# Kernel tuning notes

Hardware: AMD Instinct MI355X
Metric: run time of the kernel (lower is better)

Reference implementation:

```python
import jax, jax.numpy as jnp
import numpy as np

N = 100000      # nodes
E = 1600000     # edges
C = 128         # in_channels == hidden_dim
FP = 512        # fingerprint_dim
L = 3           # num_layers
G = 1024        # number of graphs
W_SCALE = 5.0


def setup_inputs() -> dict:
    key = jax.random.key(0)
    ks = jax.random.split(key, 6)
    x = jax.random.normal(ks[0], (N, C), dtype=jnp.float32)
    Ws = jax.random.normal(ks[1], (L, C, C), dtype=jnp.float32) * W_SCALE
    bs = jnp.zeros((L, C), dtype=jnp.float32)
    Wn = jax.random.normal(ks[2], (L, C, C), dtype=jnp.float32) * W_SCALE
    bn = jnp.zeros((L, C), dtype=jnp.float32)
    Wfp = jax.random.normal(ks[3], (L, FP, C), dtype=jnp.float32) * W_SCALE
    edge_index = jax.random.randint(ks[4], (2, E), 0, N, dtype=jnp.int64)
    batch = jnp.sort(jax.random.randint(ks[5], (N,), 0, G, dtype=jnp.int64))
    return {"x": x, "Ws": Ws, "bs": bs, "Wn": Wn, "bn": bn, "Wfp": Wfp,
            "edge_index": edge_index, "batch": batch}


def reference(x, Ws, bs, Wn, bn, Wfp, edge_index, batch):
    row, col = edge_index[0], edge_index[1]
    fingerprint = jnp.zeros((G, FP), dtype=x.dtype)
    for layer in range(L):
        # neighbor sum: scatter-add x[col] into rows (index_add)
        neigh_sum = jax.ops.segment_sum(x[col], row, num_segments=N)  # [N, C]
        x = jnp.tanh(x @ Ws[layer].T + bs[layer] + neigh_sum @ Wn[layer].T + bn[layer])
        node_contrib = jax.nn.softmax(x @ Wfp[layer].T, axis=1)  # [N, FP]
        fingerprint = fingerprint + jax.ops.segment_sum(node_contrib, batch, num_segments=G)
    return fingerprint
```

## Files before the change

### kernel.cpp

```cpp
#include <hip/hip_runtime.h>
#include <math.h>

#define NN 100000
#define EE 1600000
#define CC 128
#define FPD 512
#define GG 1024
#define LLAYERS 3
#define CAND_CAP 40
#define CAND_MARGIN 12.0f
#define BCAP 48


typedef __attribute__((ext_vector_type(8))) short short8;
typedef __attribute__((ext_vector_type(4))) float float4v;

__device__ __forceinline__ unsigned short f2bf(float f) {
  unsigned u = __float_as_uint(f);
  unsigned r = ((u >> 16) & 1u) + 0x7FFFu;
  return (unsigned short)((u + r) >> 16);
}
__device__ __forceinline__ float bf2f(unsigned short h) {
  return __uint_as_float(((unsigned)h) << 16);
}
__device__ __forceinline__ float fast_tanh(float x) {
  float e = __expf(2.0f * x);
  return 1.0f - 2.0f / (e + 1.0f);
}


#define NB_BUILD ((EE + 255) / 256)
#define NB_X ((NN * CC / 4 + 255) / 256)
#define NB_W ((LLAYERS * CC * CC / 4 + 255) / 256)
#define NB_FP ((LLAYERS * FPD * CC / 4 + 255) / 256)
#define NC_TOTAL (NB_X + 2 * NB_W + NB_FP)
#define G1 (3 * NB_BUILD)
#define NB_STARTUP (G1 + (NC_TOTAL - 2 * NB_BUILD))

__device__ __forceinline__ void conv3_body(const float* __restrict__ src,
                                           unsigned short* __restrict__ dhi,
                                           unsigned short* __restrict__ dmd,
                                           unsigned short* __restrict__ dlo,
                                           int i, int n4) {
  if (i >= n4) return;
  float4 f = ((const float4*)src)[i];
  ushort4 h, m, l;
  float r;
  h.x = f2bf(f.x); r = f.x - bf2f(h.x); m.x = f2bf(r); l.x = f2bf(r - bf2f(m.x));
  h.y = f2bf(f.y); r = f.y - bf2f(h.y); m.y = f2bf(r); l.y = f2bf(r - bf2f(m.y));
  h.z = f2bf(f.z); r = f.z - bf2f(h.z); m.z = f2bf(r); l.z = f2bf(r - bf2f(m.z));
  h.w = f2bf(f.w); r = f.w - bf2f(h.w); m.w = f2bf(r); l.w = f2bf(r - bf2f(m.w));
  ((ushort4*)dhi)[i] = h;
  ((ushort4*)dmd)[i] = m;
  ((ushort4*)dlo)[i] = l;
}

__global__ __launch_bounds__(256) void startup_kernel(
    const float* __restrict__ x, const float* __restrict__ Ws,
    const float* __restrict__ Wn, const float* __restrict__ Wfp,
    const int* __restrict__ erow, const int* __restrict__ ecol,
    unsigned short* __restrict__ xhi, unsigned short* __restrict__ xmd,
    unsigned short* __restrict__ xlo,
    unsigned short* __restrict__ wshi, unsigned short* __restrict__ wsmd,
    unsigned short* __restrict__ wslo,
    unsigned short* __restrict__ wnhi, unsigned short* __restrict__ wnmd,
    unsigned short* __restrict__ wnlo,
    unsigned short* __restrict__ wfphi,
    int* __restrict__ deg, int* __restrict__ colidx) {
  int b = blockIdx.x, t = threadIdx.x;
  int cid;
  if (b < G1) {
    int g = b / 3, r = b - g * 3;
    if (r == 2) {
      int i = g * 256 + t;
      if (i < EE) {
        int row = erow[i];
        int pos = atomicAdd(&deg[row], 1);
        if (pos < BCAP) colidx[row * BCAP + pos] = ecol[i];
      }
      return;
    }
    cid = g * 2 + r;
  } else {
    cid = 2 * NB_BUILD + (b - G1);
  }
  if (cid < NB_X) {
    conv3_body(x, xhi, xmd, xlo, cid * 256 + t, NN * CC / 4);
  } else if (cid < NB_X + NB_W) {
    conv3_body(Ws, wshi, wsmd, wslo, (cid - NB_X) * 256 + t, LLAYERS * CC * CC / 4);
  } else if (cid < NB_X + 2 * NB_W) {
    conv3_body(Wn, wnhi, wnmd, wnlo, (cid - NB_X - NB_W) * 256 + t, LLAYERS * CC * CC / 4);
  } else {
    int i = (cid - NB_X - 2 * NB_W) * 256 + t;
    int n4 = LLAYERS * FPD * CC / 4;
    if (i < n4) {
      float4 f = ((const float4*)Wfp)[i];
      ushort4 h;
      h.x = f2bf(f.x); h.y = f2bf(f.y); h.z = f2bf(f.z); h.w = f2bf(f.w);
      ((ushort4*)wfphi)[i] = h;
    }
  }
}

__device__ __forceinline__ void gather_body(const float* __restrict__ x,
                                            const int* __restrict__ deg,
                                            const int* __restrict__ colidx,
                                            unsigned short* __restrict__ axhi,
                                            unsigned short* __restrict__ axmd,
                                            unsigned short* __restrict__ axlo,
                                            int vb, int t) {
  int n = vb * 8 + (t >> 5);
  int q = t & 31;
  int dn = deg[n];
  if (dn > BCAP) dn = BCAP;
  const int* cl = colidx + n * BCAP;
  const float4* x4 = (const float4*)x;
  float4 s0 = make_float4(0.f, 0.f, 0.f, 0.f);
  float4 s1 = make_float4(0.f, 0.f, 0.f, 0.f);
  int e = 0;
  for (; e + 8 <= dn; e += 8) {
    int4 ca = ((const int4*)cl)[e >> 2];
    int4 cb = ((const int4*)cl)[(e >> 2) + 1];
    int o0 = ca.x * 32 + q, o1 = ca.y * 32 + q, o2 = ca.z * 32 + q, o3 = ca.w * 32 + q;
    int o4 = cb.x * 32 + q, o5 = cb.y * 32 + q, o6 = cb.z * 32 + q, o7 = cb.w * 32 + q;
    float4 v0 = x4[o0], v1 = x4[o1], v2 = x4[o2], v3 = x4[o3];
    float4 v4 = x4[o4], v5 = x4[o5], v6 = x4[o6], v7 = x4[o7];
    s0.x += v0.x; s0.y += v0.y; s0.z += v0.z; s0.w += v0.w;
    s1.x += v1.x; s1.y += v1.y; s1.z += v1.z; s1.w += v1.w;
    s0.x += v2.x; s0.y += v2.y; s0.z += v2.z; s0.w += v2.w;
    s1.x += v3.x; s1.y += v3.y; s1.z += v3.z; s1.w += v3.w;
    s0.x += v4.x; s0.y += v4.y; s0.z += v4.z; s0.w += v4.w;
    s1.x += v5.x; s1.y += v5.y; s1.z += v5.z; s1.w += v5.w;
    s0.x += v6.x; s0.y += v6.y; s0.z += v6.z; s0.w += v6.w;
    s1.x += v7.x; s1.y += v7.y; s1.z += v7.z; s1.w += v7.w;
  }
  if (e + 4 <= dn) {
    int4 ca = ((const int4*)cl)[e >> 2];
    int o0 = ca.x * 32 + q, o1 = ca.y * 32 + q, o2 = ca.z * 32 + q, o3 = ca.w * 32 + q;
    float4 v0 = x4[o0], v1 = x4[o1], v2 = x4[o2], v3 = x4[o3];
    s0.x += v0.x; s0.y += v0.y; s0.z += v0.z; s0.w += v0.w;
    s1.x += v1.x; s1.y += v1.y; s1.z += v1.z; s1.w += v1.w;
    s0.x += v2.x; s0.y += v2.y; s0.z += v2.z; s0.w += v2.w;
    s1.x += v3.x; s1.y += v3.y; s1.z += v3.z; s1.w += v3.w;
    e += 4;
  }
  for (; e < dn; e++) {
    int o = cl[e] * 32 + q;
    float4 v0 = x4[o];
    s0.x += v0.x; s0.y += v0.y; s0.z += v0.z; s0.w += v0.w;
  }
  float4 s = make_float4(s0.x + s1.x, s0.y + s1.y, s0.z + s1.z, s0.w + s1.w);
  ushort4 h, m, l;
  float r;
  h.x = f2bf(s.x); r = s.x - bf2f(h.x); m.x = f2bf(r); l.x = f2bf(r - bf2f(m.x));
  h.y = f2bf(s.y); r = s.y - bf2f(h.y); m.y = f2bf(r); l.y = f2bf(r - bf2f(m.y));
  h.z = f2bf(s.z); r = s.z - bf2f(h.z); m.z = f2bf(r); l.z = f2bf(r - bf2f(m.z));
  h.w = f2bf(s.w); r = s.w - bf2f(h.w); m.w = f2bf(r); l.w = f2bf(r - bf2f(m.w));
  int ob = n * CC / 4 + q;
  ((ushort4*)axhi)[ob] = h;
  ((ushort4*)axmd)[ob] = m;
  ((ushort4*)axlo)[ob] = l;
}

__global__ __launch_bounds__(256) void gather_kernel(const float* __restrict__ x,
                                                     const int* __restrict__ deg,
                                                     const int* __restrict__ colidx,
                                                     unsigned short* __restrict__ axhi,
                                                     unsigned short* __restrict__ axmd,
                                                     unsigned short* __restrict__ axlo) {
  gather_body(x, deg, colidx, axhi, axmd, axlo, blockIdx.x, threadIdx.x);
}

#define GT_SPLIT 4096
#define NBGEMM ((NN + 127) / 128)
__global__ __launch_bounds__(256, 2) void gemm_tanh_mfma(float* __restrict__ xf,
                                                         unsigned short* __restrict__ xhi,
                                                         unsigned short* __restrict__ xmd,
                                                         unsigned short* __restrict__ xlo,
                                                         const unsigned short* __restrict__ axhi,
                                                         const unsigned short* __restrict__ axmd,
                                                         const unsigned short* __restrict__ axlo,
                                                         const unsigned short* __restrict__ wshi,
                                                         const unsigned short* __restrict__ wsmd,
                                                         const unsigned short* __restrict__ wslo,
                                                         const unsigned short* __restrict__ wnhi,
                                                         const unsigned short* __restrict__ wnmd,
                                                         const unsigned short* __restrict__ wnlo,
                                                         const float* __restrict__ bsl,
                                                         const float* __restrict__ bnl) {
  __shared__ unsigned short Bsm[3 * GT_SPLIT];
  int t = threadIdx.x;
  int lane = t & 63, wv = t >> 6, quad = lane >> 4, low4 = lane & 15;
  long long nb = (long long)blockIdx.x * 128;
  int base = (int)nb + wv * 32;
  int r0 = base + low4;      if (r0 >= NN) r0 = NN - 1;
  int r1 = base + 16 + low4; if (r1 >= NN) r1 = NN - 1;
  long long a0 = (long long)r0 * CC, a1 = (long long)r1 * CC;

  float4v acc[2][8];
#pragma unroll
  for (int tl = 0; tl < 2; tl++)
#pragma unroll
    for (int t8 = 0; t8 < 8; t8++) acc[tl][t8] = (float4v)0.f;

  for (int ch = 0; ch < 8; ch++) {
    int kb = (ch & 3) * 32;
    const unsigned short* ah_ = (ch < 4) ? xhi : axhi;
    const unsigned short* am_ = (ch < 4) ? xmd : axmd;
    const unsigned short* al_ = (ch < 4) ? xlo : axlo;
    short8 ah0 = *(const short8*)(ah_ + a0 + kb + quad * 8);
    short8 am0 = *(const short8*)(am_ + a0 + kb + quad * 8);
    short8 al0 = *(const short8*)(al_ + a0 + kb + quad * 8);
    short8 ah1 = *(const short8*)(ah_ + a1 + kb + quad * 8);
    short8 am1 = *(const short8*)(am_ + a1 + kb + quad * 8);
    short8 al1 = *(const short8*)(al_ + a1 + kb + quad * 8);
    const unsigned short* bh_ = (ch < 4) ? wshi : wnhi;
    const unsigned short* bm_ = (ch < 4) ? wsmd : wnmd;
    const unsigned short* bl_ = (ch < 4) ? wslo : wnlo;
    __syncthreads();
#pragma unroll
    for (int i = 0; i < 6; i++) {
      int u = t + i * 256;
      int sp = u >> 9;
      int u2 = u & 511;
      int t8s = u2 >> 6, quads = (u2 >> 4) & 3, low4s = u2 & 15;
      int col = t8s * 16 + low4s;
      const unsigned short* bsrc = (sp == 0) ? bh_ : (sp == 1) ? bm_ : bl_;
      *(short8*)(Bsm + u * 8) = *(const short8*)(bsrc + (long long)col * CC + kb + quads * 8);
    }
    __syncthreads();
#pragma unroll
    for (int t8 = 0; t8 < 8; t8++) {
      const unsigned short* bb = Bsm + (t8 * 64 + lane) * 8;
      short8 bh = *(const short8*)(bb);
      short8 bm = *(const short8*)(bb + GT_SPLIT);
      short8 bl = *(const short8*)(bb + 2 * GT_SPLIT);
      acc[0][t8] = __builtin_amdgcn_mfma_f32_16x16x32_bf16(ah0, bh, acc[0][t8], 0, 0, 0);
      acc[1][t8] = __builtin_amdgcn_mfma_f32_16x16x32_bf16(ah1, bh, acc[1][t8], 0, 0, 0);
      acc[0][t8] = __builtin_amdgcn_mfma_f32_16x16x32_bf16(ah0, bm, acc[0][t8], 0, 0, 0);
      acc[1][t8] = __builtin_amdgcn_mfma_f32_16x16x32_bf16(ah1, bm, acc[1][t8], 0, 0, 0);
      acc[0][t8] = __builtin_amdgcn_mfma_f32_16x16x32_bf16(am0, bh, acc[0][t8], 0, 0, 0);
      acc[1][t8] = __builtin_amdgcn_mfma_f32_16x16x32_bf16(am1, bh, acc[1][t8], 0, 0, 0);
      acc[0][t8] = __builtin_amdgcn_mfma_f32_16x16x32_bf16(ah0, bl, acc[0][t8], 0, 0, 0);
      acc[1][t8] = __builtin_amdgcn_mfma_f32_16x16x32_bf16(ah1, bl, acc[1][t8], 0, 0, 0);
      acc[0][t8] = __builtin_amdgcn_mfma_f32_16x16x32_bf16(am0, bm, acc[0][t8], 0, 0, 0);
      acc[1][t8] = __builtin_amdgcn_mfma_f32_16x16x32_bf16(am1, bm, acc[1][t8], 0, 0, 0);
      acc[0][t8] = __builtin_amdgcn_mfma_f32_16x16x32_bf16(al0, bh, acc[0][t8], 0, 0, 0);
      acc[1][t8] = __builtin_amdgcn_mfma_f32_16x16x32_bf16(al1, bh, acc[1][t8], 0, 0, 0);
    }
  }

#pragma unroll
  for (int tl = 0; tl < 2; tl++)
#pragma unroll
    for (int t8 = 0; t8 < 8; t8++) {
      int c = t8 * 16 + low4;
      float b = bsl[c] + bnl[c];
#pragma unroll
      for (int r = 0; r < 4; r++) {
        long long n = nb + wv * 32 + tl * 16 + quad * 4 + r;
        if (n < NN) {
          float val = fast_tanh(acc[tl][t8][r] + b);
          unsigned short h = f2bf(val);
          float rm = val - bf2f(h);
          unsigned short m = f2bf(rm);
          xf[n * CC + c] = val;
          xhi[n * CC + c] = h;
          xmd[n * CC + c] = m;
          xlo[n * CC + c] = f2bf(rm - bf2f(m));
        }
      }
    }
}

#define FPB_SPLIT 8192
__device__ __forceinline__ void approx_refine_body(
    const unsigned short* __restrict__ xhi, const unsigned short* __restrict__ wfphi,
    const float* __restrict__ xf, const float* __restrict__ wfp,
    const int* __restrict__ batch, float* __restrict__ out,
    int vb, int t) {
  __shared__ unsigned short Bsm[FPB_SPLIT];
  __shared__ int cntsh[64];
  __shared__ unsigned short colsh[64 * CAND_CAP];
  int lane = t & 63, wv = t >> 6, quad = lane >> 4, low4 = lane & 15;
  long long nb = (long long)vb * 64;
  if (t < 64) cntsh[t] = 0;
  int rowg = (int)(nb + wv * 16 + low4);
  if (rowg >= NN) rowg = NN - 1;
  long long arow = (long long)rowg * CC;

  float m[4] = {-3.4e38f, -3.4e38f, -3.4e38f, -3.4e38f};

  for (int pass = 0; pass < 2; pass++) {
    for (int cc = 0; cc < 4; cc++) {
      float4v acc[8];
#pragma unroll
      for (int t8 = 0; t8 < 8; t8++) acc[t8] = (float4v)0.f;
      for (int kh = 0; kh < 2; kh++) {
        short8 A0 = *(const short8*)(xhi + arow + kh * 64 + quad * 8);
        short8 A1 = *(const short8*)(xhi + arow + kh * 64 + 32 + quad * 8);
        __syncthreads();
#pragma unroll
        for (int i = 0; i < 4; i++) {
          int u = t + i * 256;
          int t8s = u >> 7, sss = (u >> 6) & 1, quads = (u >> 4) & 3, low4s = u & 15;
          int col = cc * 128 + t8s * 16 + low4s;
          int kseg = sss * 4 + quads;
          *(short8*)(Bsm + u * 8) =
              *(const short8*)(wfphi + (long long)col * CC + kh * 64 + kseg * 8);
        }
        __syncthreads();
#pragma unroll
        for (int t8 = 0; t8 < 8; t8++) {
          short8 b0 = *(const short8*)(Bsm + ((t8 * 2 + 0) * 64 + lane) * 8);
          acc[t8] = __builtin_amdgcn_mfma_f32_16x16x32_bf16(A0, b0, acc[t8], 0, 0, 0);
          short8 b1 = *(const short8*)(Bsm + ((t8 * 2 + 1) * 64 + lane) * 8);
          acc[t8] = __builtin_amdgcn_mfma_f32_16x16x32_bf16(A1, b1, acc[t8], 0, 0, 0);
        }
      }
      if (pass == 0) {
#pragma unroll
        for (int r = 0; r < 4; r++)
#pragma unroll
          for (int t8 = 0; t8 < 8; t8++) m[r] = fmaxf(m[r], acc[t8][r]);
      } else {
#pragma unroll
        for (int r = 0; r < 4; r++) {
          long long rowabs = nb + wv * 16 + quad * 4 + r;
          if (rowabs >= NN) continue;
          float thr = m[r] - CAND_MARGIN;
          int rloc = wv * 16 + quad * 4 + r;
#pragma unroll
          for (int t8 = 0; t8 < 8; t8++) {
            if (acc[t8][r] > thr) {
              int idx = atomicAdd(&cntsh[rloc], 1);
              if (idx < CAND_CAP)
                colsh[rloc * CAND_CAP + idx] = (unsigned short)(cc * 128 + t8 * 16 + low4);
            }
          }
        }
      }
    }
    if (pass == 0) {
#pragma unroll
      for (int r = 0; r < 4; r++)
#pragma unroll
        for (int off = 1; off < 16; off <<= 1) m[r] = fmaxf(m[r], __shfl_xor(m[r], off, 64));
    }
  }
  __syncthreads();

  float* zsh = (float*)Bsm;
  int hw = lane >> 5, hl = lane & 31;
  for (int p8 = 0; p8 < 8; p8++) {
    int node = p8 * 8 + wv * 2 + hw;
    long long n = nb + node;
    if (n >= NN) continue;
    int cnt = cntsh[node];
    if (cnt > CAND_CAP) cnt = CAND_CAP;
    float4 xv = ((const float4*)(xf + n * CC))[hl];
    int g = batch[n];
    for (int c = 0; c < cnt; c++) {
      int j = colsh[node * CAND_CAP + c];
      float4 w4 = ((const float4*)(wfp + (long long)j * CC))[hl];
      float s = xv.x * w4.x + xv.y * w4.y + xv.z * w4.z + xv.w * w4.w;
#pragma unroll
      for (int off = 1; off < 32; off <<= 1) s += __shfl_xor(s, off, 64);
      if (hl == 0) zsh[node * CAND_CAP + c] = s;
    }
    int c0 = hl, c1 = hl + 32;
    float z0 = (c0 < cnt) ? zsh[node * CAND_CAP + c0] : -3.4e38f;
    float z1 = (c1 < cnt) ? zsh[node * CAND_CAP + c1] : -3.4e38f;
    float mz = fmaxf(z0, z1);
#pragma unroll
    for (int off = 1; off < 32; off <<= 1) mz = fmaxf(mz, __shfl_xor(mz, off, 64));
    float e0 = (c0 < cnt) ? __expf(z0 - mz) : 0.f;
    float e1 = (c1 < cnt) ? __expf(z1 - mz) : 0.f;
    float ss = e0 + e1;
#pragma unroll
    for (int off = 1; off < 32; off <<= 1) ss += __shfl_xor(ss, off, 64);
    float invs = 1.0f / ss;
    if (c0 < cnt) atomicAdd(&out[(long long)g * FPD + colsh[node * CAND_CAP + c0]], e0 * invs);
    if (c1 < cnt) atomicAdd(&out[(long long)g * FPD + colsh[node * CAND_CAP + c1]], e1 * invs);
  }
}

__global__ __launch_bounds__(256, 6) void approx_refine_kernel(
    const unsigned short* __restrict__ xhi, const unsigned short* __restrict__ wfphi,
    const float* __restrict__ xf, const float* __restrict__ wfp,
    const int* __restrict__ batch, float* __restrict__ out) {
  approx_refine_body(xhi, wfphi, xf, wfp, batch, out, blockIdx.x, threadIdx.x);
}

#define NBA ((NN + 63) / 64)
#define NBGT (NN / 8)
__global__ __launch_bounds__(256, 6) void agr_kernel(
    const unsigned short* __restrict__ xhi, const unsigned short* __restrict__ wfphi,
    const float* __restrict__ xf, const float* __restrict__ wfp,
    const int* __restrict__ batch, float* __restrict__ out,
    const int* __restrict__ deg, const int* __restrict__ colidx,
    unsigned short* __restrict__ axhi, unsigned short* __restrict__ axmd,
    unsigned short* __restrict__ axlo) {
  int b = blockIdx.x;
  int bd9 = b / 9;
  if (b - bd9 * 9 == 8) {
    approx_refine_body(xhi, wfphi, xf, wfp, batch, out, bd9, threadIdx.x);
  } else {
    int g = b - bd9;
    if (g < NBGT) gather_body(xf, deg, colidx, axhi, axmd, axlo, g, threadIdx.x);
  }
}


extern "C" void kernel_launch(void* const* d_in, const int* in_sizes, int n_in,
                              void* d_out, int out_size, void* d_ws, size_t ws_size,
                              hipStream_t stream) {
  (void)in_sizes; (void)n_in; (void)ws_size;
  const float* x   = (const float*)d_in[0];
  const float* Ws  = (const float*)d_in[1];
  const float* bs  = (const float*)d_in[2];
  const float* Wn  = (const float*)d_in[3];
  const float* bn  = (const float*)d_in[4];
  const float* Wfp = (const float*)d_in[5];
  const int*   ei  = (const int*)d_in[6];
  const int*   bat = (const int*)d_in[7];
  float* out = (float*)d_out;

  float* xf = (float*)d_ws;
  unsigned short* xhi  = (unsigned short*)(xf + (size_t)NN * CC);
  unsigned short* xmd  = xhi + (size_t)NN * CC;
  unsigned short* xlo  = xmd + (size_t)NN * CC;
  unsigned short* axhi = xlo + (size_t)NN * CC;
  unsigned short* axmd = axhi + (size_t)NN * CC;
  unsigned short* axlo = axmd + (size_t)NN * CC;
  unsigned short* wshi = axlo + (size_t)NN * CC;
  unsigned short* wsmd = wshi + (size_t)LLAYERS * CC * CC;
  unsigned short* wslo = wsmd + (size_t)LLAYERS * CC * CC;
  unsigned short* wnhi = wslo + (size_t)LLAYERS * CC * CC;
  unsigned short* wnmd = wnhi + (size_t)LLAYERS * CC * CC;
  unsigned short* wnlo = wnmd + (size_t)LLAYERS * CC * CC;
  unsigned short* wfphi = wnlo + (size_t)LLAYERS * CC * CC;
  int* deg    = (int*)(wfphi + (size_t)LLAYERS * FPD * CC);
  int* colidx = deg + NN;

  hipMemsetAsync(out, 0, (size_t)out_size * sizeof(float), stream);
  hipMemsetAsync(deg, 0, (size_t)NN * sizeof(int), stream);

  const int* erow = ei;
  const int* ecol = ei + EE;

  startup_kernel<<<NB_STARTUP, 256, 0, stream>>>(
      x, Ws, Wn, Wfp, erow, ecol,
      xhi, xmd, xlo, wshi, wsmd, wslo, wnhi, wnmd, wnlo, wfphi, deg, colidx);

  gather_kernel<<<NBGT, 256, 0, stream>>>(x, deg, colidx, axhi, axmd, axlo);

  for (int l = 0; l < LLAYERS; l++) {
    gemm_tanh_mfma<<<NBGEMM, 256, 0, stream>>>(xf, xhi, xmd, xlo, axhi, axmd, axlo,
        wshi + (size_t)l * CC * CC, wsmd + (size_t)l * CC * CC, wslo + (size_t)l * CC * CC,
        wnhi + (size_t)l * CC * CC, wnmd + (size_t)l * CC * CC, wnlo + (size_t)l * CC * CC,
        bs + (size_t)l * CC, bn + (size_t)l * CC);
    if (l < LLAYERS - 1) {
      agr_kernel<<<NBA * 9, 256, 0, stream>>>(
          xhi, wfphi + (size_t)l * FPD * CC, xf, Wfp + (size_t)l * FPD * CC,
          bat, out, deg, colidx, axhi, axmd, axlo);
    } else {
      approx_refine_kernel<<<NBA, 256, 0, stream>>>(
          xhi, wfphi + (size_t)l * FPD * CC, xf, Wfp + (size_t)l * FPD * CC, bat, out);
    }
  }
}
```

Measured before the change: 1.076 ms.

## Store activations as fp32, split to bf16 in GEMM, single-pass fingerprint scoring

Activations and neighbor sums are now kept in fp32 and split into hi/mid/lo bf16 inside the GEMM tile load. Before, three bf16 arrays were written by the startup, gather and GEMM epilogue, and the GEMM only needs to store fp32 plus the hi part. This cuts global memory traffic and removes the input conversion pass. The fingerprint scoring kernel now keeps all 512 logits in registers, so the max and candidate selection happen in one MFMA pass instead of recomputing the product twice. In exchange, register pressure is higher (launch bounds lowered to 2) and the fused gather+refine kernel is split back into separate launches, losing that overlap.

```diff
diff --git a/kernel.cpp b/kernel.cpp
--- a/kernel.cpp
+++ b/kernel.cpp
@@ -28,14 +28,25 @@
   return 1.0f - 2.0f / (e + 1.0f);
 }
 
+__device__ __forceinline__ void split3_8(const float* __restrict__ src,
+                                         short8& h8, short8& m8, short8& l8) {
+  float4 f0 = ((const float4*)src)[0];
+  float4 f1 = ((const float4*)src)[1];
+  float vv, r;
+  unsigned short h, m;
+#define SP3(idx, val)                                        \
+  vv = (val); h = f2bf(vv); r = vv - bf2f(h); m = f2bf(r);   \
+  h8[idx] = (short)h; m8[idx] = (short)m; l8[idx] = (short)f2bf(r - bf2f(m));
+  SP3(0, f0.x) SP3(1, f0.y) SP3(2, f0.z) SP3(3, f0.w)
+  SP3(4, f1.x) SP3(5, f1.y) SP3(6, f1.z) SP3(7, f1.w)
+#undef SP3
+}
+
 
 #define NB_BUILD ((EE + 255) / 256)
-#define NB_X ((NN * CC / 4 + 255) / 256)
 #define NB_W ((LLAYERS * CC * CC / 4 + 255) / 256)
 #define NB_FP ((LLAYERS * FPD * CC / 4 + 255) / 256)
-#define NC_TOTAL (NB_X + 2 * NB_W + NB_FP)
-#define G1 (3 * NB_BUILD)
-#define NB_STARTUP (G1 + (NC_TOTAL - 2 * NB_BUILD))
+#define NB_STARTUP (NB_BUILD + 2 * NB_W + NB_FP)
 
 __device__ __forceinline__ void conv3_body(const float* __restrict__ src,
                                            unsigned short* __restrict__ dhi,
@@ -56,11 +67,9 @@
 }
 
 __global__ __launch_bounds__(256) void startup_kernel(
-    const float* __restrict__ x, const float* __restrict__ Ws,
-    const float* __restrict__ Wn, const float* __restrict__ Wfp,
+    const float* __restrict__ Ws, const float* __restrict__ Wn,
+    const float* __restrict__ Wfp,
     const int* __restrict__ erow, const int* __restrict__ ecol,
-    unsigned short* __restrict__ xhi, unsigned short* __restrict__ xmd,
-    unsigned short* __restrict__ xlo,
     unsigned short* __restrict__ wshi, unsigned short* __restrict__ wsmd,
     unsigned short* __restrict__ wslo,
     unsigned short* __restrict__ wnhi, unsigned short* __restrict__ wnmd,
@@ -68,30 +77,22 @@
     unsigned short* __restrict__ wfphi,
     int* __restrict__ deg, int* __restrict__ colidx) {
   int b = blockIdx.x, t = threadIdx.x;
-  int cid;
-  if (b < G1) {
-    int g = b / 3, r = b - g * 3;
-    if (r == 2) {
-      int i = g * 256 + t;
-      if (i < EE) {
-        int row = erow[i];
-        int pos = atomicAdd(&deg[row], 1);
-        if (pos < BCAP) colidx[row * BCAP + pos] = ecol[i];
-      }
-      return;
-    }
-    cid = g * 2 + r;
+  if (b < NB_BUILD) {
+    int i = b * 256 + t;
+    if (i < EE) {
+      int row = erow[i];
+      int pos = atomicAdd(&deg[row], 1);
+      if (pos < BCAP) colidx[row * BCAP + pos] = ecol[i];
+    }
+    return;
+  }
+  int cid = b - NB_BUILD;
+  if (cid < NB_W) {
+    conv3_body(Ws, wshi, wsmd, wslo, cid * 256 + t, LLAYERS * CC * CC / 4);
+  } else if (cid < 2 * NB_W) {
+    conv3_body(Wn, wnhi, wnmd, wnlo, (cid - NB_W) * 256 + t, LLAYERS * CC * CC / 4);
   } else {
-    cid = 2 * NB_BUILD + (b - G1);
-  }
-  if (cid < NB_X) {
-    conv3_body(x, xhi, xmd, xlo, cid * 256 + t, NN * CC / 4);
-  } else if (cid < NB_X + NB_W) {
-    conv3_body(Ws, wshi, wsmd, wslo, (cid - NB_X) * 256 + t, LLAYERS * CC * CC / 4);
-  } else if (cid < NB_X + 2 * NB_W) {
-    conv3_body(Wn, wnhi, wnmd, wnlo, (cid - NB_X - NB_W) * 256 + t, LLAYERS * CC * CC / 4);
-  } else {
-    int i = (cid - NB_X - 2 * NB_W) * 256 + t;
+    int i = (cid - 2 * NB_W) * 256 + t;
     int n4 = LLAYERS * FPD * CC / 4;
     if (i < n4) {
       float4 f = ((const float4*)Wfp)[i];
@@ -102,14 +103,13 @@
   }
 }
 
-__device__ __forceinline__ void gather_body(const float* __restrict__ x,
-                                            const int* __restrict__ deg,
-                                            const int* __restrict__ colidx,
-                                            unsigned short* __restrict__ axhi,
-                                            unsigned short* __restrict__ axmd,
-                                            unsigned short* __restrict__ axlo,
-                                            int vb, int t) {
-  int n = vb * 8 + (t >> 5);
+#define NBGT (NN / 8)
+__global__ __launch_bounds__(256) void gather_kernel(const float* __restrict__ x,
+                                                     const int* __restrict__ deg,
+                                                     const int* __restrict__ colidx,
+                                                     float* __restrict__ axf) {
+  int t = threadIdx.x;
+  int n = blockIdx.x * 8 + (t >> 5);
   int q = t & 31;
   int dn = deg[n];
   if (dn > BCAP) dn = BCAP;
@@ -150,44 +150,19 @@
     s0.x += v0.x; s0.y += v0.y; s0.z += v0.z; s0.w += v0.w;
   }
   float4 s = make_float4(s0.x + s1.x, s0.y + s1.y, s0.z + s1.z, s0.w + s1.w);
-  ushort4 h, m, l;
-  float r;
-  h.x = f2bf(s.x); r = s.x - bf2f(h.x); m.x = f2bf(r); l.x = f2bf(r - bf2f(m.x));
-  h.y = f2bf(s.y); r = s.y - bf2f(h.y); m.y = f2bf(r); l.y = f2bf(r - bf2f(m.y));
-  h.z = f2bf(s.z); r = s.z - bf2f(h.z); m.z = f2bf(r); l.z = f2bf(r - bf2f(m.z));
-  h.w = f2bf(s.w); r = s.w - bf2f(h.w); m.w = f2bf(r); l.w = f2bf(r - bf2f(m.w));
-  int ob = n * CC / 4 + q;
-  ((ushort4*)axhi)[ob] = h;
-  ((ushort4*)axmd)[ob] = m;
-  ((ushort4*)axlo)[ob] = l;
-}
-
-__global__ __launch_bounds__(256) void gather_kernel(const float* __restrict__ x,
-                                                     const int* __restrict__ deg,
-                                                     const int* __restrict__ colidx,
-                                                     unsigned short* __restrict__ axhi,
-                                                     unsigned short* __restrict__ axmd,
-                                                     unsigned short* __restrict__ axlo) {
-  gather_body(x, deg, colidx, axhi, axmd, axlo, blockIdx.x, threadIdx.x);
+  ((float4*)axf)[n * 32 + q] = s;
 }
 
 #define GT_SPLIT 4096
 #define NBGEMM ((NN + 127) / 128)
-__global__ __launch_bounds__(256, 2) void gemm_tanh_mfma(float* __restrict__ xf,
-                                                         unsigned short* __restrict__ xhi,
-                                                         unsigned short* __restrict__ xmd,
-                                                         unsigned short* __restrict__ xlo,
-                                                         const unsigned short* __restrict__ axhi,
-                                                         const unsigned short* __restrict__ axmd,
-                                                         const unsigned short* __restrict__ axlo,
-                                                         const unsigned short* __restrict__ wshi,
-                                                         const unsigned short* __restrict__ wsmd,
-                                                         const unsigned short* __restrict__ wslo,
-                                                         const unsigned short* __restrict__ wnhi,
-                                                         const unsigned short* __restrict__ wnmd,
-                                                         const unsigned short* __restrict__ wnlo,
-                                                         const float* __restrict__ bsl,
-                                                         const float* __restrict__ bnl) {
+__global__ __launch_bounds__(256, 2) void gemm_tanh_mfma(
+    const float* __restrict__ xin, float* __restrict__ xf,
+    unsigned short* __restrict__ xhi, const float* __restrict__ axf,
+    const unsigned short* __restrict__ wshi, const unsigned short* __restrict__ wsmd,
+    const unsigned short* __restrict__ wslo,
+    const unsigned short* __restrict__ wnhi, const unsigned short* __restrict__ wnmd,
+    const unsigned short* __restrict__ wnlo,
+    const float* __restrict__ bsl, const float* __restrict__ bnl) {
   __shared__ unsigned short Bsm[3 * GT_SPLIT];
   int t = threadIdx.x;
   int lane = t & 63, wv = t >> 6, quad = lane >> 4, low4 = lane & 15;
@@ -205,15 +180,10 @@
 
   for (int ch = 0; ch < 8; ch++) {
     int kb = (ch & 3) * 32;
-    const unsigned short* ah_ = (ch < 4) ? xhi : axhi;
-    const unsigned short* am_ = (ch < 4) ? xmd : axmd;
-    const unsigned short* al_ = (ch < 4) ? xlo : axlo;
-    short8 ah0 = *(const short8*)(ah_ + a0 + kb + quad * 8);
-    short8 am0 = *(const short8*)(am_ + a0 + kb + quad * 8);
-    short8 al0 = *(const short8*)(al_ + a0 + kb + quad * 8);
-    short8 ah1 = *(const short8*)(ah_ + a1 + kb + quad * 8);
-    short8 am1 = *(const short8*)(am_ + a1 + kb + quad * 8);
-    short8 al1 = *(const short8*)(al_ + a1 + kb + quad * 8);
+    const float* af_ = (ch < 4) ? xin : axf;
+    short8 ah0, am0, al0, ah1, am1, al1;
+    split3_8(af_ + a0 + kb + quad * 8, ah0, am0, al0);
+    split3_8(af_ + a1 + kb + quad * 8, ah1, am1, al1);
     const unsigned short* bh_ = (ch < 4) ? wshi : wnhi;
     const unsigned short* bm_ = (ch < 4) ? wsmd : wnmd;
     const unsigned short* bl_ = (ch < 4) ? wslo : wnlo;
@@ -261,92 +231,90 @@
         long long n = nb + wv * 32 + tl * 16 + quad * 4 + r;
         if (n < NN) {
           float val = fast_tanh(acc[tl][t8][r] + b);
-          unsigned short h = f2bf(val);
-          float rm = val - bf2f(h);
-          unsigned short m = f2bf(rm);
           xf[n * CC + c] = val;
-          xhi[n * CC + c] = h;
-          xmd[n * CC + c] = m;
-          xlo[n * CC + c] = f2bf(rm - bf2f(m));
+          xhi[n * CC + c] = f2bf(val);
         }
       }
     }
 }
 
 #define FPB_SPLIT 8192
-__device__ __forceinline__ void approx_refine_body(
+#define NBA ((NN + 63) / 64)
+__global__ __launch_bounds__(256, 2) void approx_refine_kernel(
     const unsigned short* __restrict__ xhi, const unsigned short* __restrict__ wfphi,
     const float* __restrict__ xf, const float* __restrict__ wfp,
-    const int* __restrict__ batch, float* __restrict__ out,
-    int vb, int t) {
+    const int* __restrict__ batch, float* __restrict__ out) {
   __shared__ unsigned short Bsm[FPB_SPLIT];
   __shared__ int cntsh[64];
   __shared__ unsigned short colsh[64 * CAND_CAP];
+  int t = threadIdx.x;
   int lane = t & 63, wv = t >> 6, quad = lane >> 4, low4 = lane & 15;
-  long long nb = (long long)vb * 64;
+  long long nb = (long long)blockIdx.x * 64;
   if (t < 64) cntsh[t] = 0;
   int rowg = (int)(nb + wv * 16 + low4);
   if (rowg >= NN) rowg = NN - 1;
   long long arow = (long long)rowg * CC;
 
-  float m[4] = {-3.4e38f, -3.4e38f, -3.4e38f, -3.4e38f};
-
-  for (int pass = 0; pass < 2; pass++) {
+  float4v acc[4][8];
+#pragma unroll
+  for (int cc = 0; cc < 4; cc++)
+#pragma unroll
+    for (int t8 = 0; t8 < 8; t8++) acc[cc][t8] = (float4v)0.f;
+
+  for (int kh = 0; kh < 2; kh++) {
+    short8 A0 = *(const short8*)(xhi + arow + kh * 64 + quad * 8);
+    short8 A1 = *(const short8*)(xhi + arow + kh * 64 + 32 + quad * 8);
     for (int cc = 0; cc < 4; cc++) {
-      float4v acc[8];
-#pragma unroll
-      for (int t8 = 0; t8 < 8; t8++) acc[t8] = (float4v)0.f;
-      for (int kh = 0; kh < 2; kh++) {
-        short8 A0 = *(const short8*)(xhi + arow + kh * 64 + quad * 8);
-        short8 A1 = *(const short8*)(xhi + arow + kh * 64 + 32 + quad * 8);
-        __syncthreads();
-#pragma unroll
-        for (int i = 0; i < 4; i++) {
-          int u = t + i * 256;
-          int t8s = u >> 7, sss = (u >> 6) & 1, quads = (u >> 4) & 3, low4s = u & 15;
-          int col = cc * 128 + t8s * 16 + low4s;
-          int kseg = sss * 4 + quads;
-          *(short8*)(Bsm + u * 8) =
-              *(const short8*)(wfphi + (long long)col * CC + kh * 64 + kseg * 8);
-        }
-        __syncthreads();
-#pragma unroll
-        for (int t8 = 0; t8 < 8; t8++) {
-          short8 b0 = *(const short8*)(Bsm + ((t8 * 2 + 0) * 64 + lane) * 8);
-          acc[t8] = __builtin_amdgcn_mfma_f32_16x16x32_bf16(A0, b0, acc[t8], 0, 0, 0);
-          short8 b1 = *(const short8*)(Bsm + ((t8 * 2 + 1) * 64 + lane) * 8);
-          acc[t8] = __builtin_amdgcn_mfma_f32_16x16x32_bf16(A1, b1, acc[t8], 0, 0, 0);
+      __syncthreads();
+#pragma unroll
+      for (int i = 0; i < 4; i++) {
+        int u = t + i * 256;
+        int t8s = u >> 7, sss = (u >> 6) & 1, quads = (u >> 4) & 3, low4s = u & 15;
+        int col = cc * 128 + t8s * 16 + low4s;
+        int kseg = sss * 4 + quads;
+        *(short8*)(Bsm + u * 8) =
+            *(const short8*)(wfphi + (long long)col * CC + kh * 64 + kseg * 8);
+      }
+      __syncthreads();
+#pragma unroll
+      for (int t8 = 0; t8 < 8; t8++) {
+        short8 b0 = *(const short8*)(Bsm + ((t8 * 2 + 0) * 64 + lane) * 8);
+        acc[cc][t8] = __builtin_amdgcn_mfma_f32_16x16x32_bf16(A0, b0, acc[cc][t8], 0, 0, 0);
+        short8 b1 = *(const short8*)(Bsm + ((t8 * 2 + 1) * 64 + lane) * 8);
+        acc[cc][t8] = __builtin_amdgcn_mfma_f32_16x16x32_bf16(A1, b1, acc[cc][t8], 0, 0, 0);
+      }
+    }
+  }
+
+  float m[4];
+#pragma unroll
+  for (int r = 0; r < 4; r++) {
+    float mm = acc[0][0][r];
+#pragma unroll
+    for (int cc = 0; cc < 4; cc++)
+#pragma unroll
+      for (int t8 = 0; t8 < 8; t8++) mm = fmaxf(mm, acc[cc][t8][r]);
+#pragma unroll
+    for (int off = 1; off < 16; off <<= 1) mm = fmaxf(mm, __shfl_xor(mm, off, 64));
+    m[r] = mm;
+  }
+
+#pragma unroll
+  for (int r = 0; r < 4; r++) {
+    long long rowabs = nb + wv * 16 + quad * 4 + r;
+    if (rowabs >= NN) continue;
+    float thr = m[r] - CAND_MARGIN;
+    int rloc = wv * 16 + quad * 4 + r;
+#pragma unroll
+    for (int cc = 0; cc < 4; cc++)
+#pragma unroll
+      for (int t8 = 0; t8 < 8; t8++) {
+        if (acc[cc][t8][r] > thr) {
+          int idx = atomicAdd(&cntsh[rloc], 1);
+          if (idx < CAND_CAP)
+            colsh[rloc * CAND_CAP + idx] = (unsigned short)(cc * 128 + t8 * 16 + low4);
         }
       }
-      if (pass == 0) {
-#pragma unroll
-        for (int r = 0; r < 4; r++)
-#pragma unroll
-          for (int t8 = 0; t8 < 8; t8++) m[r] = fmaxf(m[r], acc[t8][r]);
-      } else {
-#pragma unroll
-        for (int r = 0; r < 4; r++) {
-          long long rowabs = nb + wv * 16 + quad * 4 + r;
-          if (rowabs >= NN) continue;
-          float thr = m[r] - CAND_MARGIN;
-          int rloc = wv * 16 + quad * 4 + r;
-#pragma unroll
-          for (int t8 = 0; t8 < 8; t8++) {
-            if (acc[t8][r] > thr) {
-              int idx = atomicAdd(&cntsh[rloc], 1);
-              if (idx < CAND_CAP)
-                colsh[rloc * CAND_CAP + idx] = (unsigned short)(cc * 128 + t8 * 16 + low4);
-            }
-          }
-        }
-      }
-    }
-    if (pass == 0) {
-#pragma unroll
-      for (int r = 0; r < 4; r++)
-#pragma unroll
-        for (int off = 1; off < 16; off <<= 1) m[r] = fmaxf(m[r], __shfl_xor(m[r], off, 64));
-    }
   }
   __syncthreads();
 
@@ -385,32 +353,6 @@
   }
 }
 
-__global__ __launch_bounds__(256, 6) void approx_refine_kernel(
-    const unsigned short* __restrict__ xhi, const unsigned short* __restrict__ wfphi,
-    const float* __restrict__ xf, const float* __restrict__ wfp,
-    const int* __restrict__ batch, float* __restrict__ out) {
-  approx_refine_body(xhi, wfphi, xf, wfp, batch, out, blockIdx.x, threadIdx.x);
-}
-
-#define NBA ((NN + 63) / 64)
-#define NBGT (NN / 8)
-__global__ __launch_bounds__(256, 6) void agr_kernel(
-    const unsigned short* __restrict__ xhi, const unsigned short* __restrict__ wfphi,
-    const float* __restrict__ xf, const float* __restrict__ wfp,
-    const int* __restrict__ batch, float* __restrict__ out,
-    const int* __restrict__ deg, const int* __restrict__ colidx,
-    unsigned short* __restrict__ axhi, unsigned short* __restrict__ axmd,
-    unsigned short* __restrict__ axlo) {
-  int b = blockIdx.x;
-  int bd9 = b / 9;
-  if (b - bd9 * 9 == 8) {
-    approx_refine_body(xhi, wfphi, xf, wfp, batch, out, bd9, threadIdx.x);
-  } else {
-    int g = b - bd9;
-    if (g < NBGT) gather_body(xf, deg, colidx, axhi, axmd, axlo, g, threadIdx.x);
-  }
-}
-
 
 extern "C" void kernel_launch(void* const* d_in, const int* in_sizes, int n_in,
                               void* d_out, int out_size, void* d_ws, size_t ws_size,
@@ -426,14 +368,10 @@
   const int*   bat = (const int*)d_in[7];
   float* out = (float*)d_out;
 
-  float* xf = (float*)d_ws;
-  unsigned short* xhi  = (unsigned short*)(xf + (size_t)NN * CC);
-  unsigned short* xmd  = xhi + (size_t)NN * CC;
-  unsigned short* xlo  = xmd + (size_t)NN * CC;
-  unsigned short* axhi = xlo + (size_t)NN * CC;
-  unsigned short* axmd = axhi + (size_t)NN * CC;
-  unsigned short* axlo = axmd + (size_t)NN * CC;
-  unsigned short* wshi = axlo + (size_t)NN * CC;
+  float* xf  = (float*)d_ws;
+  float* axf = xf + (size_t)NN * CC;
+  unsigned short* xhi  = (unsigned short*)(axf + (size_t)NN * CC);
+  unsigned short* wshi = xhi + (size_t)NN * CC;
   unsigned short* wsmd = wshi + (size_t)LLAYERS * CC * CC;
   unsigned short* wslo = wsmd + (size_t)LLAYERS * CC * CC;
   unsigned short* wnhi = wslo + (size_t)LLAYERS * CC * CC;
@@ -450,23 +388,21 @@
   const int* ecol = ei + EE;
 
   startup_kernel<<<NB_STARTUP, 256, 0, stream>>>(
-      x, Ws, Wn, Wfp, erow, ecol,
-      xhi, xmd, xlo, wshi, wsmd, wslo, wnhi, wnmd, wnlo, wfphi, deg, colidx);
-
-  gather_kernel<<<NBGT, 256, 0, stream>>>(x, deg, colidx, axhi, axmd, axlo);
+      Ws, Wn, Wfp, erow, ecol,
+      wshi, wsmd, wslo, wnhi, wnmd, wnlo, wfphi, deg, colidx);
+
+  gather_kernel<<<NBGT, 256, 0, stream>>>(x, deg, colidx, axf);
 
   for (int l = 0; l < LLAYERS; l++) {
-    gemm_tanh_mfma<<<NBGEMM, 256, 0, stream>>>(xf, xhi, xmd, xlo, axhi, axmd, axlo,
+    const float* xin = (l == 0) ? x : xf;
+    gemm_tanh_mfma<<<NBGEMM, 256, 0, stream>>>(
+        xin, xf, xhi, axf,
         wshi + (size_t)l * CC * CC, wsmd + (size_t)l * CC * CC, wslo + (size_t)l * CC * CC,
         wnhi + (size_t)l * CC * CC, wnmd + (size_t)l * CC * CC, wnlo + (size_t)l * CC * CC,
         bs + (size_t)l * CC, bn + (size_t)l * CC);
-    if (l < LLAYERS - 1) {
-      agr_kernel<<<NBA * 9, 256, 0, stream>>>(
-          xhi, wfphi + (size_t)l * FPD * CC, xf, Wfp + (size_t)l * FPD * CC,
-          bat, out, deg, colidx, axhi, axmd, axlo);
-    } else {
-      approx_refine_kernel<<<NBA, 256, 0, stream>>>(
-          xhi, wfphi + (size_t)l * FPD * CC, xf, Wfp + (size_t)l * FPD * CC, bat, out);
-    }
-  }
-}
+    if (l < LLAYERS - 1)
+      gather_kernel<<<NBGT, 256, 0, stream>>>(xf, deg, colidx, axf);
+    approx_refine_kernel<<<NBA, 256, 0, stream>>>(
+        xhi, wfphi + (size_t)l * FPD * CC, xf, Wfp + (size_t)l * FPD * CC, bat, out);
+  }
+}
```

Result: slower. 1.139 ms (+5.8%).
